# Performance work log

Hardware: AMD Instinct MI355X
Metric: run time of the kernel (lower is better)

Reference implementation:

```python
import jax, jax.numpy as jnp
import numpy as np

ANCHORS = np.array([[10.0, 13.0], [16.0, 30.0], [33.0, 23.0]], dtype=np.float32)
IMG_DIM = 608
NUM_CLASS = 80


def setup_inputs() -> dict:
    key = jax.random.key(0)
    nB, nA, nH, nW = 32, 3, 76, 76
    attrib = 5 + NUM_CLASS  # 85
    x = jax.random.normal(key, (nB, nA * attrib, nH, nW), dtype=jnp.float32)
    return {"x": x}


def reference(x):
    nB, C, nH, nW = x.shape
    nA = ANCHORS.shape[0]
    attrib = 5 + NUM_CLASS
    stride = IMG_DIM / nH  # 8.0
    anchors = jnp.asarray(ANCHORS) / stride  # [nA, 2] in grid units

    # [nB, nA, nH, nW, attrib]
    preds = x.reshape(nB, nA, attrib, nH, nW).transpose(0, 1, 3, 4, 2)

    # mesh grid of cell offsets: mesh_x varies along W, mesh_y along H
    mesh_x = jnp.arange(nW, dtype=x.dtype)[None, :]   # [1, nW]
    mesh_y = jnp.arange(nH, dtype=x.dtype)[:, None]   # [nH, 1]

    xy = jax.nn.sigmoid(preds[..., 0:2])
    bx = xy[..., 0] + mesh_x                            # broadcast over [nB,nA,nH,nW]
    by = xy[..., 1] + mesh_y
    wh = jnp.exp(preds[..., 2:4]) * anchors[None, :, None, None, :]

    conf = jax.nn.sigmoid(preds[..., 4:5])
    cls = jax.nn.sigmoid(preds[..., 5:])

    boxes = jnp.stack([bx, by], axis=-1)
    boxes = jnp.concatenate([boxes, wh], axis=-1) * stride  # [nB,nA,nH,nW,4]

    out = jnp.concatenate([boxes, conf, cls], axis=-1)      # [nB,nA,nH,nW,attrib]
    # permute(0,2,3,1,4) then flatten -> [nB, nH*nW*nA, attrib]
    out = out.transpose(0, 2, 3, 1, 4).reshape(nB, nA * nH * nW, attrib)
    return out
```

## Files before the change

kernel.cpp:

```cpp
#include <hip/hip_runtime.h>


typedef float f4 __attribute__((ext_vector_type(4)));

constexpr int NB = 32;
constexpr int NH = 76;
constexpr int NW = 76;
constexpr int C = 255;
constexpr int ROW_F4 = NW / 4;
constexpr int BLK_F4 = C * ROW_F4;
constexpr int TILES = NB * NH;
constexpr int NTH = 1024;
constexpr int KMAX = 5;
constexpr int TAIL = BLK_F4 - 4 * NTH;
constexpr int GRID = 512;
constexpr int NXCD = 8;
constexpr int PER_XCD = TILES / NXCD;
constexpr int BLKS_PER_XCD = GRID / NXCD;
constexpr float STRIDE = 8.0f;

__global__ __launch_bounds__(NTH, 8) void yolo_kernel(const f4* __restrict__ x4,
                                                      f4* __restrict__ out4) {
    __shared__ f4 buf[BLK_F4];
    float* __restrict__ tb = (float*)buf;

    const int tid = threadIdx.x;

    int offk[KMAX];
#pragma unroll
    for (int k = 0; k < KMAX; ++k) {
        const int i = tid + k * NTH;
        const int ii = (k < 4 || tid < TAIL) ? i : 0;
        const int row = ii / ROW_F4;
        const int c = ii - row * ROW_F4;
        offk[k] = row * (NH * ROW_F4) + c;
    }

    const int x = blockIdx.x & (NXCD - 1);
    const int j = blockIdx.x >> 3;
    const int base_t = x * PER_XCD;
    const int ntile = 4 + (j < (PER_XCD - 4 * BLKS_PER_XCD) ? 1 : 0);

    f4 stage[KMAX];

    auto issue = [&](int t) {
        const int b = t / NH;
        const int h = t - b * NH;
        const size_t inb = (size_t)b * (C * NH * ROW_F4) + (size_t)h * ROW_F4;
#pragma unroll
        for (int k = 0; k < KMAX; ++k)
            if (k < 4 || tid < TAIL) stage[k] = x4[inb + offk[k]];
    };

    int t = base_t + j;
    issue(t);
    int idx = 0;

    while (true) {
        const float hf = (float)(t % NH);

        if (idx > 0) __syncthreads();

#pragma unroll
        for (int k = 0; k < KMAX; ++k) {
            if (!(k < 4 || tid < TAIL)) continue;
            const int i = tid + k * NTH;
            const int row = i / ROW_F4;
            const int c = i - row * ROW_F4;
            const int a = (row >= 85 ? 1 : 0) + (row >= 170 ? 1 : 0);
            const int attr = row - 85 * a;
            const bool m3 = (attr == 2) || (attr == 3);
            const bool m12 = attr < 2;
            const float aw = (a == 0) ? 10.f : ((a == 1) ? 16.f : 33.f);
            const float ah = (a == 0) ? 13.f : ((a == 1) ? 30.f : 23.f);
            const float aux3 = (attr == 2) ? aw : ah;
            const float w0 = (float)(4 * c);
            const int base = 4 * c * C + row;

            const f4 v = stage[k];
            f4 r;
#pragma unroll
            for (int e = 0; e < 4; ++e) {
                const float ve = v[e];
                const float E = __expf(m3 ? ve : -ve);
                const float sg = 1.0f / (1.0f + E);
                const float add = (attr == 0) ? (w0 + (float)e) : hf;
                float o = m3 ? (E * aux3) : sg;
                if (m12) o = (sg + add) * STRIDE;
                r[e] = o;
            }
            tb[base]         = r.x;
            tb[base + C]     = r.y;
            tb[base + 2 * C] = r.z;
            tb[base + 3 * C] = r.w;
        }

        const size_t ob = (size_t)t * BLK_F4;
        ++idx;
        const bool more = (idx < ntile);
        if (more) {
            t = base_t + idx * BLKS_PER_XCD + j;
            issue(t);
        }

        __syncthreads();

#pragma unroll
        for (int k = 0; k < KMAX; ++k) {
            const int i = tid + k * NTH;
            if (k < 4 || tid < TAIL)
                __builtin_nontemporal_store(buf[i], &out4[ob + i]);
        }

        if (!more) break;
    }
}

extern "C" void kernel_launch(void* const* d_in, const int* in_sizes, int n_in,
                              void* d_out, int out_size, void* d_ws, size_t ws_size,
                              hipStream_t stream) {
    const f4* x4 = (const f4*)d_in[0];
    f4* out4 = (f4*)d_out;
    yolo_kernel<<<GRID, NTH, 0, stream>>>(x4, out4);
}
```

Baseline: 63.81 us.

## Split each tile into two column halves and pipeline transpose with stores

Each (batch,row) tile is split into two column halves, w in [0,40) and [40,76), each with its own LDS buffer. The loop interleaves loading, transforming and storing the halves so one half's global stores overlap the other half's transform. This removes the full-block serialization between the LDS transpose and the store phase. In exchange the per-half division by 10 or 9 makes loads narrower per row, and an extra barrier is added per tile.

```diff
diff --git a/kernel.cpp b/kernel.cpp
--- a/kernel.cpp
+++ b/kernel.cpp
@@ -3,70 +3,76 @@
 
 typedef float f4 __attribute__((ext_vector_type(4)));
 
-constexpr int NB = 32;
+constexpr int NBATCH = 32;
 constexpr int NH = 76;
 constexpr int NW = 76;
 constexpr int C = 255;
 constexpr int ROW_F4 = NW / 4;
 constexpr int BLK_F4 = C * ROW_F4;
-constexpr int TILES = NB * NH;
+constexpr int TILES = NBATCH * NH;
 constexpr int NTH = 1024;
-constexpr int KMAX = 5;
-constexpr int TAIL = BLK_F4 - 4 * NTH;
 constexpr int GRID = 512;
 constexpr int NXCD = 8;
 constexpr int PER_XCD = TILES / NXCD;
-constexpr int BLKS_PER_XCD = GRID / NXCD;
+constexpr int BPX = GRID / NXCD;
 constexpr float STRIDE = 8.0f;
+
+constexpr int AF4 = 2550;
+constexpr int BF4 = 2295;
+constexpr int TAILA = AF4 - 2 * NTH;
+constexpr int TAILB = BF4 - 2 * NTH;
 
 __global__ __launch_bounds__(NTH, 8) void yolo_kernel(const f4* __restrict__ x4,
                                                       f4* __restrict__ out4) {
-    __shared__ f4 buf[BLK_F4];
-    float* __restrict__ tb = (float*)buf;
+    __shared__ f4 bufA[AF4];
+    __shared__ f4 bufB[BF4];
+    float* __restrict__ tA = (float*)bufA;
+    float* __restrict__ tB = (float*)bufB;
 
     const int tid = threadIdx.x;
-
-    int offk[KMAX];
-#pragma unroll
-    for (int k = 0; k < KMAX; ++k) {
-        const int i = tid + k * NTH;
-        const int ii = (k < 4 || tid < TAIL) ? i : 0;
-        const int row = ii / ROW_F4;
-        const int c = ii - row * ROW_F4;
-        offk[k] = row * (NH * ROW_F4) + c;
-    }
 
     const int x = blockIdx.x & (NXCD - 1);
     const int j = blockIdx.x >> 3;
     const int base_t = x * PER_XCD;
-    const int ntile = 4 + (j < (PER_XCD - 4 * BLKS_PER_XCD) ? 1 : 0);
+    const int ntile = 4 + (j < (PER_XCD - 4 * BPX) ? 1 : 0);
 
-    f4 stage[KMAX];
+    f4 stA[3], stB[3];
 
-    auto issue = [&](int t) {
+    auto issueA = [&](int t) {
         const int b = t / NH;
         const int h = t - b * NH;
         const size_t inb = (size_t)b * (C * NH * ROW_F4) + (size_t)h * ROW_F4;
 #pragma unroll
-        for (int k = 0; k < KMAX; ++k)
-            if (k < 4 || tid < TAIL) stage[k] = x4[inb + offk[k]];
+        for (int k = 0; k < 3; ++k) {
+            if (k == 2 && tid >= TAILA) continue;
+            const int i = tid + k * NTH;
+            const int row = i / 10;
+            const int cl = i - row * 10;
+            stA[k] = x4[inb + (size_t)row * (NH * ROW_F4) + cl];
+        }
+    };
+    auto issueB = [&](int t) {
+        const int b = t / NH;
+        const int h = t - b * NH;
+        const size_t inb = (size_t)b * (C * NH * ROW_F4) + (size_t)h * ROW_F4;
+#pragma unroll
+        for (int k = 0; k < 3; ++k) {
+            if (k == 2 && tid >= TAILB) continue;
+            const int i = tid + k * NTH;
+            const int row = i / 9;
+            const int cl = i - row * 9;
+            stB[k] = x4[inb + (size_t)row * (NH * ROW_F4) + cl + 10];
+        }
     };
 
-    int t = base_t + j;
-    issue(t);
-    int idx = 0;
-
-    while (true) {
+    auto xsA = [&](int t) {
         const float hf = (float)(t % NH);
-
-        if (idx > 0) __syncthreads();
-
 #pragma unroll
-        for (int k = 0; k < KMAX; ++k) {
-            if (!(k < 4 || tid < TAIL)) continue;
+        for (int k = 0; k < 3; ++k) {
+            if (k == 2 && tid >= TAILA) continue;
             const int i = tid + k * NTH;
-            const int row = i / ROW_F4;
-            const int c = i - row * ROW_F4;
+            const int row = i / 10;
+            const int cl = i - row * 10;
             const int a = (row >= 85 ? 1 : 0) + (row >= 170 ? 1 : 0);
             const int attr = row - 85 * a;
             const bool m3 = (attr == 2) || (attr == 3);
@@ -74,10 +80,9 @@
             const float aw = (a == 0) ? 10.f : ((a == 1) ? 16.f : 33.f);
             const float ah = (a == 0) ? 13.f : ((a == 1) ? 30.f : 23.f);
             const float aux3 = (attr == 2) ? aw : ah;
-            const float w0 = (float)(4 * c);
-            const int base = 4 * c * C + row;
-
-            const f4 v = stage[k];
+            const float w0 = (float)(4 * cl);
+            const int base = 4 * cl * C + row;
+            const f4 v = stA[k];
             f4 r;
 #pragma unroll
             for (int e = 0; e < 4; ++e) {
@@ -89,30 +94,93 @@
                 if (m12) o = (sg + add) * STRIDE;
                 r[e] = o;
             }
-            tb[base]         = r.x;
-            tb[base + C]     = r.y;
-            tb[base + 2 * C] = r.z;
-            tb[base + 3 * C] = r.w;
+            tA[base]         = r.x;
+            tA[base + C]     = r.y;
+            tA[base + 2 * C] = r.z;
+            tA[base + 3 * C] = r.w;
         }
+    };
+    auto xsB = [&](int t) {
+        const float hf = (float)(t % NH);
+#pragma unroll
+        for (int k = 0; k < 3; ++k) {
+            if (k == 2 && tid >= TAILB) continue;
+            const int i = tid + k * NTH;
+            const int row = i / 9;
+            const int cl = i - row * 9;
+            const int a = (row >= 85 ? 1 : 0) + (row >= 170 ? 1 : 0);
+            const int attr = row - 85 * a;
+            const bool m3 = (attr == 2) || (attr == 3);
+            const bool m12 = attr < 2;
+            const float aw = (a == 0) ? 10.f : ((a == 1) ? 16.f : 33.f);
+            const float ah = (a == 0) ? 13.f : ((a == 1) ? 30.f : 23.f);
+            const float aux3 = (attr == 2) ? aw : ah;
+            const float w0 = (float)(4 * (cl + 10));
+            const int base = 4 * cl * C + row;
+            const f4 v = stB[k];
+            f4 r;
+#pragma unroll
+            for (int e = 0; e < 4; ++e) {
+                const float ve = v[e];
+                const float E = __expf(m3 ? ve : -ve);
+                const float sg = 1.0f / (1.0f + E);
+                const float add = (attr == 0) ? (w0 + (float)e) : hf;
+                float o = m3 ? (E * aux3) : sg;
+                if (m12) o = (sg + add) * STRIDE;
+                r[e] = o;
+            }
+            tB[base]         = r.x;
+            tB[base + C]     = r.y;
+            tB[base + 2 * C] = r.z;
+            tB[base + 3 * C] = r.w;
+        }
+    };
 
+    auto storeA = [&](int t) {
         const size_t ob = (size_t)t * BLK_F4;
-        ++idx;
-        const bool more = (idx < ntile);
-        if (more) {
-            t = base_t + idx * BLKS_PER_XCD + j;
-            issue(t);
+#pragma unroll
+        for (int k = 0; k < 3; ++k) {
+            const int i = tid + k * NTH;
+            if (k < 2 || i < AF4)
+                __builtin_nontemporal_store(bufA[i], &out4[ob + i]);
         }
+    };
+    auto storeB = [&](int t) {
+        const size_t ob = (size_t)t * BLK_F4 + AF4;
+#pragma unroll
+        for (int k = 0; k < 3; ++k) {
+            const int i = tid + k * NTH;
+            if (k < 2 || i < BF4)
+                __builtin_nontemporal_store(bufB[i], &out4[ob + i]);
+        }
+    };
 
+    int ti = 0;
+    int t = base_t + j;
+    issueA(t);
+    issueB(t);
+    xsA(t);
+    __syncthreads();
+
+    while (true) {
+        const bool more = (ti + 1 < ntile);
+        const int tn = more ? (base_t + (ti + 1) * BPX + j) : 0;
+
+        if (more) issueA(tn);
+        xsB(t);
+        storeA(t);
         __syncthreads();
 
-#pragma unroll
-        for (int k = 0; k < KMAX; ++k) {
-            const int i = tid + k * NTH;
-            if (k < 4 || tid < TAIL)
-                __builtin_nontemporal_store(buf[i], &out4[ob + i]);
+        if (more) {
+            issueB(tn);
+            xsA(tn);
         }
+        storeB(t);
+        if (!more) break;
+        __syncthreads();
 
-        if (!more) break;
+        t = tn;
+        ++ti;
     }
 }
 
```

Measured after the change: 103.6 us. +62.4%, slower.

## Split LDS tile into two halves to overlap scatter with global stores

Applied to the files above, without the earlier changes.

The output tile in shared memory is split into an A half (columns c<10, the first 2550 float4) and a B half. Scattering one half now runs while the other half is being stored, and the next tile's load is issued in between, so global stores overlap with compute and loads instead of running after a full barrier. The cost is more complex control flow and the same number of barriers per tile, each guarding only half the data.

```diff
diff --git a/kernel.cpp b/kernel.cpp
--- a/kernel.cpp
+++ b/kernel.cpp
@@ -3,20 +3,24 @@
 
 typedef float f4 __attribute__((ext_vector_type(4)));
 
-constexpr int NB = 32;
+constexpr int NBATCH = 32;
 constexpr int NH = 76;
 constexpr int NW = 76;
 constexpr int C = 255;
 constexpr int ROW_F4 = NW / 4;
 constexpr int BLK_F4 = C * ROW_F4;
-constexpr int TILES = NB * NH;
+constexpr int TILES = NBATCH * NH;
 constexpr int NTH = 1024;
 constexpr int KMAX = 5;
 constexpr int TAIL = BLK_F4 - 4 * NTH;
 constexpr int GRID = 512;
 constexpr int NXCD = 8;
 constexpr int PER_XCD = TILES / NXCD;
-constexpr int BLKS_PER_XCD = GRID / NXCD;
+constexpr int BPX = GRID / NXCD;
+constexpr int AF4 = 2550;
+constexpr int BF4 = BLK_F4 - AF4;
+constexpr int TAILA = AF4 - 2 * NTH;
+constexpr int TAILB = BF4 - 2 * NTH;
 constexpr float STRIDE = 8.0f;
 
 __global__ __launch_bounds__(NTH, 8) void yolo_kernel(const f4* __restrict__ x4,
@@ -39,7 +43,7 @@
     const int x = blockIdx.x & (NXCD - 1);
     const int j = blockIdx.x >> 3;
     const int base_t = x * PER_XCD;
-    const int ntile = 4 + (j < (PER_XCD - 4 * BLKS_PER_XCD) ? 1 : 0);
+    const int ntile = 4 + (j < (PER_XCD - 4 * BPX) ? 1 : 0);
 
     f4 stage[KMAX];
 
@@ -52,21 +56,15 @@
             if (k < 4 || tid < TAIL) stage[k] = x4[inb + offk[k]];
     };
 
-    int t = base_t + j;
-    issue(t);
-    int idx = 0;
-
-    while (true) {
+    auto scatter = [&](int t, bool selB) {
         const float hf = (float)(t % NH);
-
-        if (idx > 0) __syncthreads();
-
 #pragma unroll
         for (int k = 0; k < KMAX; ++k) {
             if (!(k < 4 || tid < TAIL)) continue;
             const int i = tid + k * NTH;
             const int row = i / ROW_F4;
             const int c = i - row * ROW_F4;
+            if (selB ? (c < 10) : (c >= 10)) continue;
             const int a = (row >= 85 ? 1 : 0) + (row >= 170 ? 1 : 0);
             const int attr = row - 85 * a;
             const bool m3 = (attr == 2) || (attr == 3);
@@ -94,25 +92,53 @@
             tb[base + 2 * C] = r.z;
             tb[base + 3 * C] = r.w;
         }
+    };
 
+    auto storeA = [&](int t) {
         const size_t ob = (size_t)t * BLK_F4;
-        ++idx;
-        const bool more = (idx < ntile);
-        if (more) {
-            t = base_t + idx * BLKS_PER_XCD + j;
-            issue(t);
+#pragma unroll
+        for (int k = 0; k < 3; ++k) {
+            const int i = tid + k * NTH;
+            if (k < 2 || tid < TAILA)
+                __builtin_nontemporal_store(buf[i], &out4[ob + i]);
+        }
+    };
+    auto storeB = [&](int t) {
+        const size_t ob = (size_t)t * BLK_F4 + AF4;
+#pragma unroll
+        for (int k = 0; k < 3; ++k) {
+            const int i = tid + k * NTH;
+            if (k < 2 || tid < TAILB)
+                __builtin_nontemporal_store(buf[AF4 + i], &out4[ob + i]);
+        }
+    };
+
+    int t = base_t + j;
+    issue(t);
+    scatter(t, false);
+    __syncthreads();
+
+    int idx = 0;
+    while (true) {
+        const bool more = (idx + 1 < ntile);
+        const int tn = more ? (base_t + (idx + 1) * BPX + j) : 0;
+
+        scatter(t, true);
+        if (more) issue(tn);
+        storeA(t);
+        __syncthreads();
+
+        if (!more) {
+            storeB(t);
+            break;
         }
 
+        scatter(tn, false);
+        storeB(t);
         __syncthreads();
 
-#pragma unroll
-        for (int k = 0; k < KMAX; ++k) {
-            const int i = tid + k * NTH;
-            if (k < 4 || tid < TAIL)
-                __builtin_nontemporal_store(buf[i], &out4[ob + i]);
-        }
-
-        if (!more) break;
+        t = tn;
+        ++idx;
     }
 }
 
```

New measurement: 70.72 us. 10.8% more time.
